# Kernel tuning notes

Measured on AMD Instinct MI355X. Metric: run time of the kernel, lower is better.

The kernel has to match this reference:

```python
import jax, jax.numpy as jnp
import numpy as np

N = 100_000
E = 1_600_000
F_IN = 14
H = 64
N_BLOCKS = 105
N_STEMS_OUT = 105
S = 10_000
KEEP = 0.8  # 1 - drop_prob


def setup_inputs() -> dict:
    key = jax.random.key(0)
    ks = jax.random.split(key, 16)
    x = jax.random.normal(ks[0], (N, F_IN), dtype=jnp.float32)
    edge_index = jax.random.randint(ks[1], (2, E), 0, N, dtype=jnp.int64)
    stem_idxs = jax.random.randint(ks[2], (S,), 0, N, dtype=jnp.int64)
    # learned params (glorot-ish init)
    W1 = jax.random.normal(ks[3], (F_IN + 1, H), dtype=jnp.float32) / np.sqrt(F_IN + 1)
    b1 = jnp.zeros((H,), dtype=jnp.float32)
    W2 = jax.random.normal(ks[4], (H, H), dtype=jnp.float32) / np.sqrt(H)
    b2 = jnp.zeros((H,), dtype=jnp.float32)
    Wb = jax.random.normal(ks[5], (H, N_BLOCKS), dtype=jnp.float32) / np.sqrt(H)
    bb = jnp.zeros((N_BLOCKS,), dtype=jnp.float32)
    Ws = jax.random.normal(ks[6], (H, N_STEMS_OUT), dtype=jnp.float32) / np.sqrt(H)
    bs = jnp.zeros((N_STEMS_OUT,), dtype=jnp.float32)
    # inverted-dropout masks (deterministic reference for F.dropout(p=0.2))
    drop1 = (jax.random.bernoulli(ks[7], KEEP, (N, H)).astype(jnp.float32)) / KEEP
    drop2 = (jax.random.bernoulli(ks[8], KEEP, (N, H)).astype(jnp.float32)) / KEEP
    # gumbel noise g = -log(-log(U)) for gumbel_softmax(tau=1, hard=False)
    u1 = jax.random.uniform(ks[9], (N, N_BLOCKS), minval=1e-10, maxval=1.0)
    u2 = jax.random.uniform(ks[10], (N, N_STEMS_OUT), minval=1e-10, maxval=1.0)
    gb = -jnp.log(-jnp.log(u1)).astype(jnp.float32)
    gs = -jnp.log(-jnp.log(u2)).astype(jnp.float32)
    return {"x": x, "W1": W1, "b1": b1, "W2": W2, "b2": b2,
            "Wb": Wb, "bb": bb, "Ws": Ws, "bs": bs,
            "drop1": drop1, "drop2": drop2, "gb": gb, "gs": gs,
            "edge_index": edge_index, "stem_idxs": stem_idxs}


def gcn_conv(x, W, b, src, dst, norm, n):
    """PyG GCNConv (normalize=True, self-loops already appended in src/dst/norm)."""
    xw = x @ W                                    # [n, out]
    msg = xw[src] * norm[:, None]                 # gather + scale  [E+n, out]
    out = jax.ops.segment_sum(msg, dst, num_segments=n)  # scatter-add
    return out + b


def _gcn_norm(edge_index, n):
    # append self loops, edge weight 1; symmetric normalization
    loops = jnp.arange(n, dtype=edge_index.dtype)
    src = jnp.concatenate([edge_index[0], loops])
    dst = jnp.concatenate([edge_index[1], loops])
    deg = jax.ops.segment_sum(jnp.ones_like(dst, dtype=jnp.float32), dst, num_segments=n)
    dis = jnp.where(deg > 0, jax.lax.rsqrt(deg), 0.0)
    norm = dis[src] * dis[dst]
    return src, dst, norm


def reference(x, W1, b1, W2, b2, Wb, bb, Ws, bs, drop1, drop2, gb, gs, edge_index, stem_idxs):
    n = x.shape[0]
    stem_feature = jnp.zeros((n,), dtype=x.dtype).at[stem_idxs].set(1.0)
    h = jnp.concatenate([x, stem_feature[:, None]], axis=1)  # [N, F_IN+1]
    src, dst, norm = _gcn_norm(edge_index, n)
    h = jax.nn.relu(gcn_conv(h, W1, b1, src, dst, norm, n)) * drop1
    h = jax.nn.relu(gcn_conv(h, W2, b2, src, dst, norm, n)) * drop2
    block_logits = h @ Wb + bb
    stem_logits = h @ Ws + bs
    selected_block = jax.nn.softmax(block_logits + gb, axis=-1)  # gumbel_softmax tau=1 soft
    selected_stem = jax.nn.softmax(stem_logits + gs, axis=-1)
    return (block_logits, stem_logits, selected_block, selected_stem)
```

## Files before the change

kernel.cpp:

```cpp
#include <hip/hip_runtime.h>
#include <hip/hip_bf16.h>
#include <math.h>

#define N_NODES 100000
#define N_EDGES 1600000
#define FIN 14
#define H 64
#define NB 105
#define S_CNT 10000
#define SCAN_BLOCKS 391
#define NBKT 391
#define BBLK 250
#define EPB 6400

__global__ __launch_bounds__(256) void deg_kernel(const int* __restrict__ dst,
                                                  int* __restrict__ deg) {
    int e = blockIdx.x * 256 + threadIdx.x;
    atomicAdd(&deg[dst[e]], 1);
}

__global__ __launch_bounds__(256) void stem_kernel(const int* __restrict__ idx,
                                                   float* __restrict__ stem01) {
    int i = blockIdx.x * 256 + threadIdx.x;
    if (i < S_CNT) stem01[idx[i]] = 1.0f;
}

__global__ __launch_bounds__(256) void dis_kernel(const int* __restrict__ deg,
                                                  float* __restrict__ dis) {
    int i = blockIdx.x * 256 + threadIdx.x;
    if (i < N_NODES) dis[i] = rsqrtf((float)deg[i] + 1.0f);
}

__global__ __launch_bounds__(256) void scan1_kernel(const int* __restrict__ deg,
                                                    int* __restrict__ rowptr,
                                                    int* __restrict__ bsum) {
    __shared__ int s[256];
    int t = threadIdx.x;
    int i = blockIdx.x * 256 + t;
    int v = (i < N_NODES) ? deg[i] : 0;
    s[t] = v;
    __syncthreads();
#pragma unroll
    for (int o = 1; o < 256; o <<= 1) {
        int x = (t >= o) ? s[t - o] : 0;
        __syncthreads();
        s[t] += x;
        __syncthreads();
    }
    if (i < N_NODES) rowptr[i + 1] = s[t];
    if (t == 255) bsum[blockIdx.x] = s[255];
}

__global__ __launch_bounds__(512) void scan2_kernel(const int* __restrict__ bsum,
                                                    int* __restrict__ boff) {
    __shared__ int s[512];
    int t = threadIdx.x;
    int v = (t < SCAN_BLOCKS) ? bsum[t] : 0;
    s[t] = v;
    __syncthreads();
#pragma unroll
    for (int o = 1; o < 512; o <<= 1) {
        int x = (t >= o) ? s[t - o] : 0;
        __syncthreads();
        s[t] += x;
        __syncthreads();
    }
    if (t < SCAN_BLOCKS) boff[t] = s[t] - v;
}

__global__ __launch_bounds__(256) void scan3_kernel(const int* __restrict__ boff,
                                                    int* __restrict__ rowptr) {
    int t = threadIdx.x;
    int i = blockIdx.x * 256 + t;
    if (i < N_NODES) rowptr[i + 1] += boff[blockIdx.x];
    if (i == 0) rowptr[0] = 0;
}

__global__ __launch_bounds__(256) void bincnt_kernel(const int* __restrict__ dst,
                                                     int* __restrict__ hist) {
    __shared__ int lh[NBKT];
    int t = threadIdx.x;
    for (int i = t; i < NBKT; i += 256) lh[i] = 0;
    __syncthreads();
    int e0 = blockIdx.x * EPB;
    for (int i = t; i < EPB; i += 256) atomicAdd(&lh[dst[e0 + i] >> 8], 1);
    __syncthreads();
    for (int i = t; i < NBKT; i += 256) hist[i * BBLK + blockIdx.x] = lh[i];
}

__global__ __launch_bounds__(256) void binscan_kernel(int* __restrict__ hist,
                                                      const int* __restrict__ rowptr) {
    __shared__ int s[256];
    int t = threadIdx.x, b = blockIdx.x;
    int v = (t < BBLK) ? hist[b * BBLK + t] : 0;
    s[t] = v;
    __syncthreads();
#pragma unroll
    for (int o = 1; o < 256; o <<= 1) {
        int x = (t >= o) ? s[t - o] : 0;
        __syncthreads();
        s[t] += x;
        __syncthreads();
    }
    if (t < BBLK) hist[b * BBLK + t] = rowptr[b * 256] + s[t] - v;
}

__global__ __launch_bounds__(256) void binscat_kernel(const int* __restrict__ src,
                                                      const int* __restrict__ dst,
                                                      const int* __restrict__ hist,
                                                      int* __restrict__ tmp) {
    __shared__ int lofs[NBKT];
    __shared__ int lcnt[NBKT];
    int t = threadIdx.x;
    for (int i = t; i < NBKT; i += 256) {
        lofs[i] = hist[i * BBLK + blockIdx.x];
        lcnt[i] = 0;
    }
    __syncthreads();
    int e0 = blockIdx.x * EPB;
    for (int i = t; i < EPB; i += 256) {
        int s = src[e0 + i], d = dst[e0 + i];
        int b = d >> 8;
        int r = atomicAdd(&lcnt[b], 1);
        tmp[lofs[b] + r] = s | ((d & 255) << 17);
    }
}

__global__ __launch_bounds__(256) void bsort_kernel(const int* __restrict__ tmp,
                                                    const int* __restrict__ rowptr,
                                                    int* __restrict__ col) {
    __shared__ int cur[256];
    int t = threadIdx.x, b = blockIdx.x;
    int n0 = b * 256;
    int idx = n0 + t;
    cur[t] = (idx < N_NODES) ? rowptr[idx] : 0;
    __syncthreads();
    int beg = rowptr[n0];
    int nend = n0 + 256; if (nend > N_NODES) nend = N_NODES;
    int end = rowptr[nend];
    for (int i = beg + t; i < end; i += 256) {
        int p = tmp[i];
        int pos = atomicAdd(&cur[p >> 17], 1);
        col[pos] = p & 0x1FFFF;
    }
}

__global__ __launch_bounds__(256) void wpadT_kernel(const float* __restrict__ Wb,
                                                    const float* __restrict__ Ws,
                                                    float* __restrict__ WpT) {
    int i = blockIdx.x * 256 + threadIdx.x;
    if (i < 224 * 64) {
        int c = i >> 6, k = i & 63;
        float w = 0.f;
        if (c < NB) w = Wb[k * NB + c];
        else if (c >= 112 && c < 112 + NB) w = Ws[k * NB + (c - 112)];
        WpT[i] = w;
    }
}

__global__ __launch_bounds__(256) void xw1_kernel(const float* __restrict__ x,
                                                  const float* __restrict__ stem01,
                                                  const float* __restrict__ dis,
                                                  const float* __restrict__ W1,
                                                  float* __restrict__ xws) {
    __shared__ __align__(16) float W1s[15 * 64];
    __shared__ __align__(16) float xs[4][16];
    int tid = threadIdx.x;
    for (int i = tid; i < 960; i += 256) W1s[i] = W1[i];
    int n0 = blockIdx.x * 4;
    if (tid < 60) {
        int r = tid / 15, k = tid % 15;
        int n = n0 + r;
        xs[r][k] = (k < FIN) ? x[n * FIN + k] : stem01[n];
    }
    __syncthreads();
    int r = tid >> 6, f = tid & 63;
    float acc = 0.f;
#pragma unroll
    for (int k = 0; k < 15; k++) acc += xs[r][k] * W1s[k * 64 + f];
    xws[(n0 + r) * 64 + f] = acc * dis[n0 + r];
}

__global__ __launch_bounds__(256) void agg_csr_kernel(const float* __restrict__ xws,
                                                      const int* __restrict__ rowptr,
                                                      const int* __restrict__ col,
                                                      const float* __restrict__ dis,
                                                      const float* __restrict__ bias,
                                                      const float* __restrict__ drop,
                                                      float* __restrict__ hout) {
    int node = (blockIdx.x * 256 + threadIdx.x) >> 6;
    int f = threadIdx.x & 63;
    int beg = rowptr[node], end = rowptr[node + 1];
    float acc0 = xws[node * 64 + f];
    float acc1 = 0.f, acc2 = 0.f, acc3 = 0.f;
    int j = beg;
    for (; j + 4 <= end; j += 4) {
        int s0 = col[j], s1 = col[j + 1], s2 = col[j + 2], s3 = col[j + 3];
        acc0 += xws[s0 * 64 + f];
        acc1 += xws[s1 * 64 + f];
        acc2 += xws[s2 * 64 + f];
        acc3 += xws[s3 * 64 + f];
    }
    for (; j < end; j++) acc0 += xws[col[j] * 64 + f];
    float acc = (acc0 + acc1) + (acc2 + acc3);
    float r = fmaxf(fmaf(dis[node], acc, bias[f]), 0.f) * drop[node * 64 + f];
    hout[node * 64 + f] = r;
}

__global__ __launch_bounds__(256) void xw2_kernel(const float* __restrict__ h,
                                                  const float* __restrict__ dis,
                                                  const float* __restrict__ W2,
                                                  float* __restrict__ xws) {
    __shared__ __align__(16) float W2s[64 * 64];
    __shared__ __align__(16) float hsT[64 * 68];
    int tid = threadIdx.x;
    for (int i = tid; i < 4096; i += 256) W2s[i] = W2[i];
    int n0 = blockIdx.x * 64;
    for (int i = tid; i < 4096; i += 256) {
        int m = i >> 6, k = i & 63;
        int n = n0 + m;
        hsT[k * 68 + m] = (n < N_NODES) ? h[n * 64 + k] : 0.f;
    }
    __syncthreads();
    int fg = tid & 15, mg = tid >> 4;
    int f0 = fg * 4, m0 = mg * 4;
    float acc[4][4];
#pragma unroll
    for (int i = 0; i < 4; i++)
#pragma unroll
        for (int j = 0; j < 4; j++) acc[i][j] = 0.f;
    for (int k = 0; k < 64; k++) {
        float4 w = *(const float4*)&W2s[k * 64 + f0];
        float4 hv = *(const float4*)&hsT[k * 68 + m0];
        float hh[4] = {hv.x, hv.y, hv.z, hv.w};
#pragma unroll
        for (int i = 0; i < 4; i++) {
            acc[i][0] += hh[i] * w.x;
            acc[i][1] += hh[i] * w.y;
            acc[i][2] += hh[i] * w.z;
            acc[i][3] += hh[i] * w.w;
        }
    }
#pragma unroll
    for (int i = 0; i < 4; i++) {
        int n = n0 + m0 + i;
        if (n < N_NODES) {
            float ds = dis[n];
            float4 r = make_float4(acc[i][0] * ds, acc[i][1] * ds,
                                   acc[i][2] * ds, acc[i][3] * ds);
            *(float4*)&xws[n * 64 + f0] = r;
        }
    }
}

__global__ __launch_bounds__(256) void fhead_kernel(const float* __restrict__ h2,
                                                    const float* __restrict__ WpT,
                                                    const float* __restrict__ bb,
                                                    const float* __restrict__ bs,
                                                    const float* __restrict__ gb,
                                                    const float* __restrict__ gs,
                                                    float* __restrict__ out) {
    __shared__ __align__(16) float hl[4][16 * 64];
    const size_t NA = (size_t)N_NODES * NB;
    int tid = threadIdx.x;
    int widx = tid >> 6, lane = tid & 63;
    int wid = blockIdx.x * 4 + widx;
    int n0 = wid * 16;
    if (n0 >= N_NODES) return;
    int half = lane >> 5;
    int lp = lane & 31;

    {
        const float4* src = (const float4*)(h2 + (size_t)n0 * 64);
        float4* dstp = (float4*)hl[widx];
#pragma unroll
        for (int q = 0; q < 4; q++) dstp[q * 64 + lane] = src[q * 64 + lane];
    }

    int hoff = half * 112;
    const float* bias = half ? bs : bb;
    const float* g = half ? gs : gb;
    bool v3 = (lp + 96) < NB;
    int c3 = v3 ? (lp + 96) : 104;
    const float* w0p = WpT + (size_t)(hoff + lp) * 64;
    const float* w1p = WpT + (size_t)(hoff + lp + 32) * 64;
    const float* w2p = WpT + (size_t)(hoff + lp + 64) * 64;
    const float* w3p = WpT + (size_t)(hoff + c3) * 64;
    float bv0 = bias[lp], bv1 = bias[lp + 32], bv2 = bias[lp + 64];
    float bv3 = v3 ? bias[lp + 96] : 0.f;

    float acc[16][4];
#pragma unroll
    for (int j = 0; j < 16; j++)
#pragma unroll
        for (int r = 0; r < 4; r++) acc[j][r] = 0.f;

    const float* hw = hl[widx];
    float4 w0 = *(const float4*)&w0p[0];
    float4 w1 = *(const float4*)&w1p[0];
    float4 w2 = *(const float4*)&w2p[0];
    float4 w3 = *(const float4*)&w3p[0];
    for (int k4 = 0; k4 < 16; k4++) {
        int kn = (k4 < 15) ? (k4 + 1) * 4 : 60;
        float4 nw0 = *(const float4*)&w0p[kn];
        float4 nw1 = *(const float4*)&w1p[kn];
        float4 nw2 = *(const float4*)&w2p[kn];
        float4 nw3 = *(const float4*)&w3p[kn];
#pragma unroll
        for (int j = 0; j < 16; j++) {
            float4 hq = *(const float4*)&hw[j * 64 + k4 * 4];
            acc[j][0] += hq.x * w0.x + hq.y * w0.y + hq.z * w0.z + hq.w * w0.w;
            acc[j][1] += hq.x * w1.x + hq.y * w1.y + hq.z * w1.z + hq.w * w1.w;
            acc[j][2] += hq.x * w2.x + hq.y * w2.y + hq.z * w2.z + hq.w * w2.w;
            acc[j][3] += hq.x * w3.x + hq.y * w3.y + hq.z * w3.z + hq.w * w3.w;
        }
        w0 = nw0; w1 = nw1; w2 = nw2; w3 = nw3;
    }

#pragma unroll
    for (int j = 0; j < 16; j++) {
        int n = n0 + j;
        const float* gr = g + (size_t)n * NB;
        float l0 = acc[j][0] + bv0;
        float l1 = acc[j][1] + bv1;
        float l2 = acc[j][2] + bv2;
        float l3 = acc[j][3] + bv3;
        float z0 = l0 + gr[lp];
        float z1 = l1 + gr[lp + 32];
        float z2 = l2 + gr[lp + 64];
        float z3 = v3 ? (l3 + gr[lp + 96]) : -INFINITY;
        float m = fmaxf(fmaxf(z0, z1), fmaxf(z2, z3));
#pragma unroll
        for (int off = 16; off; off >>= 1) m = fmaxf(m, __shfl_xor(m, off));
        float e0 = __expf(z0 - m);
        float e1 = __expf(z1 - m);
        float e2 = __expf(z2 - m);
        float e3 = v3 ? __expf(z3 - m) : 0.f;
        float s = (e0 + e1) + (e2 + e3);
#pragma unroll
        for (int off = 16; off; off >>= 1) s += __shfl_xor(s, off);
        float inv = 1.f / s;
        float* lo = out + (size_t)half * NA + (size_t)n * NB;
        float* so = lo + 2 * NA;
        lo[lp] = l0; lo[lp + 32] = l1; lo[lp + 64] = l2;
        so[lp] = e0 * inv; so[lp + 32] = e1 * inv; so[lp + 64] = e2 * inv;
        if (v3) { lo[lp + 96] = l3; so[lp + 96] = e3 * inv; }
    }
}

extern "C" void kernel_launch(void* const* d_in, const int* in_sizes, int n_in,
                              void* d_out, int out_size, void* d_ws, size_t ws_size,
                              hipStream_t stream) {
    const float* x     = (const float*)d_in[0];
    const float* W1    = (const float*)d_in[1];
    const float* b1    = (const float*)d_in[2];
    const float* W2    = (const float*)d_in[3];
    const float* b2    = (const float*)d_in[4];
    const float* Wb    = (const float*)d_in[5];
    const float* bb    = (const float*)d_in[6];
    const float* Ws    = (const float*)d_in[7];
    const float* bs    = (const float*)d_in[8];
    const float* drop1 = (const float*)d_in[9];
    const float* drop2 = (const float*)d_in[10];
    const float* gb    = (const float*)d_in[11];
    const float* gs    = (const float*)d_in[12];
    const int* edge    = (const int*)d_in[13];
    const int* stem    = (const int*)d_in[14];
    float* out = (float*)d_out;

    float* A      = (float*)d_ws;
    float* B      = A + (size_t)N_NODES * 64;
    float* dis    = B + (size_t)N_NODES * 64;
    float* stem01 = dis + N_NODES;
    int*   deg    = (int*)(stem01 + N_NODES);
    int*   rowptr = deg + N_NODES;
    int*   hist   = rowptr + (N_NODES + 1);
    int*   bsum   = hist + N_NODES;
    int*   boff   = bsum + SCAN_BLOCKS;
    int*   col    = boff + SCAN_BLOCKS;
    float* WpT    = (float*)(col + N_EDGES);
    int*   tmp    = (int*)d_out;

    const int* esrc = edge;
    const int* edst = edge + N_EDGES;

    hipMemsetAsync(deg, 0, N_NODES * sizeof(int), stream);
    hipMemsetAsync(stem01, 0, N_NODES * sizeof(float), stream);

    deg_kernel<<<N_EDGES / 256, 256, 0, stream>>>(edst, deg);
    stem_kernel<<<(S_CNT + 255) / 256, 256, 0, stream>>>(stem, stem01);
    dis_kernel<<<SCAN_BLOCKS, 256, 0, stream>>>(deg, dis);
    wpadT_kernel<<<(224 * 64 + 255) / 256, 256, 0, stream>>>(Wb, Ws, WpT);

    scan1_kernel<<<SCAN_BLOCKS, 256, 0, stream>>>(deg, rowptr, bsum);
    scan2_kernel<<<1, 512, 0, stream>>>(bsum, boff);
    scan3_kernel<<<SCAN_BLOCKS, 256, 0, stream>>>(boff, rowptr);

    bincnt_kernel<<<BBLK, 256, 0, stream>>>(edst, hist);
    binscan_kernel<<<NBKT, 256, 0, stream>>>(hist, rowptr);
    binscat_kernel<<<BBLK, 256, 0, stream>>>(esrc, edst, hist, tmp);
    bsort_kernel<<<NBKT, 256, 0, stream>>>(tmp, rowptr, col);

    xw1_kernel<<<N_NODES / 4, 256, 0, stream>>>(x, stem01, dis, W1, A);
    agg_csr_kernel<<<(N_NODES * 64) / 256, 256, 0, stream>>>(A, rowptr, col, dis, b1, drop1, B);

    xw2_kernel<<<(N_NODES + 63) / 64, 256, 0, stream>>>(B, dis, W2, B);
    agg_csr_kernel<<<(N_NODES * 64) / 256, 256, 0, stream>>>(B, rowptr, col, dis, b2, drop2, A);

    fhead_kernel<<<(N_NODES / 16 + 3) / 4, 256, 0, stream>>>(A, WpT, bb, bs, gb, gs, out);
}
```

Before: 738.1 us.

## Split fused head into logits GEMM kernel and separate gumbel-softmax kernel

Splits the fused head kernel in two. The first computes only the block and stem logits, with 8 nodes per wave instead of 16 and no weight prefetch. The second re-reads those logits together with the gumbel noise and computes the softmax, using one wave per node and head. The aim is to cut register pressure and raise occupancy in the GEMM, and to make the softmax loads and stores coalesced, at the cost of an extra read of the logits from global memory and one more kernel launch.

```diff
diff --git a/kernel.cpp b/kernel.cpp
--- a/kernel.cpp
+++ b/kernel.cpp
@@ -253,33 +253,29 @@
     }
 }
 
-__global__ __launch_bounds__(256) void fhead_kernel(const float* __restrict__ h2,
-                                                    const float* __restrict__ WpT,
-                                                    const float* __restrict__ bb,
-                                                    const float* __restrict__ bs,
-                                                    const float* __restrict__ gb,
-                                                    const float* __restrict__ gs,
-                                                    float* __restrict__ out) {
-    __shared__ __align__(16) float hl[4][16 * 64];
+__global__ __launch_bounds__(256) void hlog_kernel(const float* __restrict__ h2,
+                                                   const float* __restrict__ WpT,
+                                                   const float* __restrict__ bb,
+                                                   const float* __restrict__ bs,
+                                                   float* __restrict__ out) {
+    __shared__ __align__(16) float hl[4][8 * 64];
     const size_t NA = (size_t)N_NODES * NB;
     int tid = threadIdx.x;
     int widx = tid >> 6, lane = tid & 63;
     int wid = blockIdx.x * 4 + widx;
-    int n0 = wid * 16;
-    if (n0 >= N_NODES) return;
+    int n0 = wid * 8;
     int half = lane >> 5;
     int lp = lane & 31;
 
     {
         const float4* src = (const float4*)(h2 + (size_t)n0 * 64);
         float4* dstp = (float4*)hl[widx];
-#pragma unroll
-        for (int q = 0; q < 4; q++) dstp[q * 64 + lane] = src[q * 64 + lane];
+        dstp[lane] = src[lane];
+        dstp[64 + lane] = src[64 + lane];
     }
 
     int hoff = half * 112;
     const float* bias = half ? bs : bb;
-    const float* g = half ? gs : gb;
     bool v3 = (lp + 96) < NB;
     int c3 = v3 ? (lp + 96) : 104;
     const float* w0p = WpT + (size_t)(hoff + lp) * 64;
@@ -289,63 +285,65 @@
     float bv0 = bias[lp], bv1 = bias[lp + 32], bv2 = bias[lp + 64];
     float bv3 = v3 ? bias[lp + 96] : 0.f;
 
-    float acc[16][4];
-#pragma unroll
-    for (int j = 0; j < 16; j++)
+    float acc[8][4];
+#pragma unroll
+    for (int j = 0; j < 8; j++)
 #pragma unroll
         for (int r = 0; r < 4; r++) acc[j][r] = 0.f;
 
     const float* hw = hl[widx];
-    float4 w0 = *(const float4*)&w0p[0];
-    float4 w1 = *(const float4*)&w1p[0];
-    float4 w2 = *(const float4*)&w2p[0];
-    float4 w3 = *(const float4*)&w3p[0];
+#pragma unroll 4
     for (int k4 = 0; k4 < 16; k4++) {
-        int kn = (k4 < 15) ? (k4 + 1) * 4 : 60;
-        float4 nw0 = *(const float4*)&w0p[kn];
-        float4 nw1 = *(const float4*)&w1p[kn];
-        float4 nw2 = *(const float4*)&w2p[kn];
-        float4 nw3 = *(const float4*)&w3p[kn];
-#pragma unroll
-        for (int j = 0; j < 16; j++) {
+        float4 w0 = *(const float4*)&w0p[k4 * 4];
+        float4 w1 = *(const float4*)&w1p[k4 * 4];
+        float4 w2 = *(const float4*)&w2p[k4 * 4];
+        float4 w3 = *(const float4*)&w3p[k4 * 4];
+#pragma unroll
+        for (int j = 0; j < 8; j++) {
             float4 hq = *(const float4*)&hw[j * 64 + k4 * 4];
             acc[j][0] += hq.x * w0.x + hq.y * w0.y + hq.z * w0.z + hq.w * w0.w;
             acc[j][1] += hq.x * w1.x + hq.y * w1.y + hq.z * w1.z + hq.w * w1.w;
             acc[j][2] += hq.x * w2.x + hq.y * w2.y + hq.z * w2.z + hq.w * w2.w;
             acc[j][3] += hq.x * w3.x + hq.y * w3.y + hq.z * w3.z + hq.w * w3.w;
         }
-        w0 = nw0; w1 = nw1; w2 = nw2; w3 = nw3;
-    }
-
-#pragma unroll
-    for (int j = 0; j < 16; j++) {
-        int n = n0 + j;
-        const float* gr = g + (size_t)n * NB;
-        float l0 = acc[j][0] + bv0;
-        float l1 = acc[j][1] + bv1;
-        float l2 = acc[j][2] + bv2;
-        float l3 = acc[j][3] + bv3;
-        float z0 = l0 + gr[lp];
-        float z1 = l1 + gr[lp + 32];
-        float z2 = l2 + gr[lp + 64];
-        float z3 = v3 ? (l3 + gr[lp + 96]) : -INFINITY;
-        float m = fmaxf(fmaxf(z0, z1), fmaxf(z2, z3));
-#pragma unroll
-        for (int off = 16; off; off >>= 1) m = fmaxf(m, __shfl_xor(m, off));
-        float e0 = __expf(z0 - m);
-        float e1 = __expf(z1 - m);
-        float e2 = __expf(z2 - m);
-        float e3 = v3 ? __expf(z3 - m) : 0.f;
-        float s = (e0 + e1) + (e2 + e3);
-#pragma unroll
-        for (int off = 16; off; off >>= 1) s += __shfl_xor(s, off);
-        float inv = 1.f / s;
-        float* lo = out + (size_t)half * NA + (size_t)n * NB;
-        float* so = lo + 2 * NA;
-        lo[lp] = l0; lo[lp + 32] = l1; lo[lp + 64] = l2;
-        so[lp] = e0 * inv; so[lp + 32] = e1 * inv; so[lp + 64] = e2 * inv;
-        if (v3) { lo[lp + 96] = l3; so[lp + 96] = e3 * inv; }
-    }
+    }
+
+    float* ob = out + (size_t)half * NA + (size_t)n0 * NB;
+#pragma unroll
+    for (int j = 0; j < 8; j++) {
+        float* lo = ob + (size_t)j * NB;
+        lo[lp] = acc[j][0] + bv0;
+        lo[lp + 32] = acc[j][1] + bv1;
+        lo[lp + 64] = acc[j][2] + bv2;
+        if (v3) lo[lp + 96] = acc[j][3] + bv3;
+    }
+}
+
+__global__ __launch_bounds__(256) void gsm_kernel(const float* __restrict__ gb,
+                                                  const float* __restrict__ gs,
+                                                  float* __restrict__ out) {
+    const size_t NA = (size_t)N_NODES * NB;
+    int wid = blockIdx.x * 4 + (threadIdx.x >> 6);
+    int lane = threadIdx.x & 63;
+    int n = wid >> 1;
+    if (n >= N_NODES) return;
+    int head = wid & 1;
+    const float* L = out + (head ? NA : 0) + (size_t)n * NB;
+    const float* g = (head ? gs : gb) + (size_t)n * NB;
+    float z0 = L[lane] + g[lane];
+    float z1 = (lane < NB - 64) ? L[lane + 64] + g[lane + 64] : -INFINITY;
+    float m = fmaxf(z0, z1);
+#pragma unroll
+    for (int off = 32; off; off >>= 1) m = fmaxf(m, __shfl_xor(m, off));
+    float e0 = __expf(z0 - m);
+    float e1 = (lane < NB - 64) ? __expf(z1 - m) : 0.f;
+    float s = e0 + e1;
+#pragma unroll
+    for (int off = 32; off; off >>= 1) s += __shfl_xor(s, off);
+    float inv = 1.f / s;
+    float* o = out + (2 + head) * NA + (size_t)n * NB;
+    o[lane] = e0 * inv;
+    if (lane < NB - 64) o[lane + 64] = e1 * inv;
 }
 
 extern "C" void kernel_launch(void* const* d_in, const int* in_sizes, int n_in,
@@ -407,5 +405,6 @@
     xw2_kernel<<<(N_NODES + 63) / 64, 256, 0, stream>>>(B, dis, W2, B);
     agg_csr_kernel<<<(N_NODES * 64) / 256, 256, 0, stream>>>(B, rowptr, col, dis, b2, drop2, A);
 
-    fhead_kernel<<<(N_NODES / 16 + 3) / 4, 256, 0, stream>>>(A, WpT, bb, bs, gb, gs, out);
-}
+    hlog_kernel<<<N_NODES / 8 / 4, 256, 0, stream>>>(A, WpT, bb, bs, out);
+    gsm_kernel<<<(2 * N_NODES) / 4, 256, 0, stream>>>(gb, gs, out);
+}
```

Measured after the change: 729.4 us. Within noise of the previous version (-1.2%).
